# Kernel optimization log

Measured on AMD Instinct MI355X. Metric: run time of the kernel, lower is better.

## Reference

```python
import jax, jax.numpy as jnp
import numpy as np
from jax import lax

# 4D convolution via lax.conv_general_dilated (supports N spatial dims natively)
# Layout: x is (N, C, T, U, V, W); weight is (O, I, kT, kU, kV, kW)

def conv4d(x, w, b):
    dn = lax.conv_dimension_numbers(x.shape, w.shape, ('NCTUVW', 'OITUVW', 'NCTUVW'))
    y = lax.conv_general_dilated(x, w, window_strides=(1, 1, 1, 1), padding='SAME',
                                 dimension_numbers=dn)
    return y + b[None, :, None, None, None, None]


def setup_inputs() -> dict:
    key = jax.random.key(0)
    k0, k1, k2, k3, k4 = jax.random.split(key, 5)
    B, C_in, C_hid, C_out = 2, 64, 128, 64
    T, D, H, W = 4, 16, 32, 32
    K = 3  # kernel size per dim (stmode 'C' -> (3,3,3,3))
    x = jax.random.normal(k0, (B, C_in, T, D, H, W), dtype=jnp.float32)
    scale1 = 1.0 / np.sqrt(C_in * K ** 4)
    scale2 = 1.0 / np.sqrt(C_hid * K ** 4)
    w1 = jax.random.normal(k1, (C_hid, C_in, K, K, K, K), dtype=jnp.float32) * scale1
    b1 = jax.random.normal(k2, (C_hid,), dtype=jnp.float32) * scale1
    w2 = jax.random.normal(k3, (C_out, C_hid, K, K, K, K), dtype=jnp.float32) * scale2
    b2 = jax.random.normal(k4, (C_out,), dtype=jnp.float32) * scale2
    return {"x": x, "w1": w1, "b1": b1, "w2": w2, "b2": b2}


def reference(x, w1, b1, w2, b2):
    # conv1 -> ReLU -> (dropout p=0 is identity) -> conv2 -> (dropout identity)
    h = jax.nn.relu(conv4d(x, w1, b1))
    return conv4d(h, w2, b2)
```

## Files before the change

kernel.cpp:

```cpp
#include <hip/hip_runtime.h>


using bf16x8 = __attribute__((ext_vector_type(8))) __bf16;
using f32x16 = __attribute__((ext_vector_type(16))) float;
using f32x4  = __attribute__((ext_vector_type(4))) float;

typedef __attribute__((address_space(1))) const void as1_void;
typedef __attribute__((address_space(3))) void as3_void;
__device__ __forceinline__ void gload_lds16(const void* g, void* l) {
    __builtin_amdgcn_global_load_lds((as1_void*)g, (as3_void*)l, 16, 0, 0);
}

__global__ __launch_bounds__(256) void cvt_x(const float* __restrict__ x,
                                             __bf16* __restrict__ x_t,
                                             __bf16* __restrict__ zp) {
    __shared__ float lt[64][65];
    if (blockIdx.x == 0 && blockIdx.y == 0)
        *(uint4*)((char*)zp + threadIdx.x * 16) = make_uint4(0u, 0u, 0u, 0u);
    const int nb = blockIdx.y;
    const int p0 = blockIdx.x * 64;
    const int tu = p0 >> 10;
    const float* src = x + (size_t)nb * 64 * 65536;
    __bf16* dst = x_t + (size_t)nb * 65536 * 64;
    #pragma unroll
    for (int i = 0; i < 16; ++i) {
        int idx = i * 256 + threadIdx.x;
        int c = idx >> 6, p = idx & 63;
        lt[c][p] = src[(size_t)c * 65536 + p0 + p];
    }
    __syncthreads();
    #pragma unroll
    for (int it = 0; it < 2; ++it) {
        int idx = it * 256 + threadIdx.x;
        int pl = idx & 63;
        int chunk = idx >> 6;
        int p = p0 + pl;
        int v = (p >> 5) & 31, w = p & 31;
        bf16x8 pk;
        #pragma unroll
        for (int e = 0; e < 8; ++e)
            pk[e] = (__bf16)lt[chunk * 8 + e][pl];
        *(bf16x8*)(dst + (size_t)(tu * 32 + v) * 2048 + chunk * 256 + w * 8) = pk;
    }
}

template <int CIN>
__global__ __launch_bounds__(256) void cvt_w(const float* __restrict__ w,
                                             __bf16* __restrict__ wt) {
    constexpr int COUT = 8192 / CIN;
    constexpr int LOGC = (CIN == 64) ? 7 : 6;
    const int tap = blockIdx.x;
    __bf16* dst = wt + (size_t)tap * 8192;
    #pragma unroll
    for (int it = 0; it < 32; ++it) {
        const int i  = it * 256 + threadIdx.x;
        const int cl = i & 15;
        const int o  = (i >> 4) & (COUT - 1);
        const int kg = i >> (4 + LOGC);
        dst[i] = (__bf16)w[(size_t)(o * CIN + kg * 16 + cl) * 81 + tap];
    }
}

template <int CIN, int COUT, int NSPLIT, bool RELU>
__global__ __launch_bounds__(128, 2) void conv4d_mfma(
    const __bf16* __restrict__ in_t,
    const __bf16* __restrict__ wt,
    const float* __restrict__ bias,
    __bf16* __restrict__ out_bf,
    float* __restrict__ out_f,
    const __bf16* __restrict__ zpage)
{
    constexpr int KST     = CIN / 16;
    constexpr int UNITS   = CIN / 32;
    constexpr int LOGU    = (UNITS == 2) ? 1 : 2;
    constexpr int SLOTS   = 6 * 136;
    constexpr int SLOTS_P = 896;
    constexpr int RNDS    = 7;
    constexpr int BUFB_P  = SLOTS_P * 16;

    __shared__ __bf16 tile[2 * SLOTS_P * 8];

    const int tid  = threadIdx.x;
    const int lane = tid & 63;
    const int l31  = lane & 31;
    const int hl   = lane >> 5;
    const int wv   = tid >> 6;

    const int bid = blockIdx.x;
    const int xcd = bid & 7;
    const int s0  = bid >> 3;
    const int u   = xcd * 2 + (s0 & 1);
    const int vg  = (s0 >> 1) & 7;
    const int t   = (s0 >> 4) & 3;
    const int nb  = (s0 >> 6) & 1;
    const int nsp = (s0 >> 7) & (NSPLIT - 1);
    const int v0  = vg * 4;
    const int pbase = ((t * 16 + u) * 32 + v0) * 32;

    const __bf16* inb = in_t + (size_t)nb * 65536 * CIN;

    int goff[RNDS];
    #pragma unroll
    for (int r = 0; r < RNDS; ++r) {
        const int slot = r * 128 + tid;
        const int row  = slot / 136;
        const int rem  = slot - row * 136;
        const int chunk = rem / 34;
        const int wp   = rem - chunk * 34;
        const int v_in = v0 - 1 + row;
        const int w_in = wp - 1;
        const bool ok = (slot < SLOTS) && ((unsigned)v_in < 32u) &&
                        ((unsigned)w_in < 32u);
        goff[r] = ok ? (v_in * (CIN * 32) + chunk * 256 + w_in * 8) : -1;
    }

    const int lane_base = hl * 34 + l31;
    const bf16x8* tile16 = (const bf16x8*)tile;

    const int o = nsp * 64 + wv * 32 + l31;
    const __bf16* wlane = wt + (size_t)o * 16 + hl * 8;

    int sb[9], tb0[9], nst = 0;
    #pragma unroll
    for (int kt = 0; kt < 3; ++kt) {
        const int t_in = t + kt - 1;
        if ((unsigned)t_in >= 4u) continue;
        #pragma unroll
        for (int ku = 0; ku < 3; ++ku) {
            const int u_in = u + ku - 1;
            if ((unsigned)u_in >= 16u) continue;
            sb[nst]  = (t_in * 16 + u_in) * 1024 * CIN;
            tb0[nst] = (kt * 3 + ku) * 9;
            ++nst;
        }
    }
    const int U = nst * UNITS;

    f32x16 acc[4];
    #pragma unroll
    for (int mt = 0; mt < 4; ++mt)
        #pragma unroll
        for (int i = 0; i < 16; ++i)
            acc[mt][i] = 0.f;

    auto issue = [&](int buf, int j) {
        const int st = j >> LOGU, ch = j & (UNITS - 1);
        const __bf16* gb = inb + sb[st] + ch * 1024;
        char* lb = ((char*)tile) + buf * BUFB_P + wv * 1024;
        #pragma unroll
        for (int r = 0; r < RNDS; ++r) {
            const __bf16* ga = (goff[r] >= 0) ? gb + goff[r] : zpage;
            gload_lds16(ga, lb + r * 2048);
        }
    };

    auto ldA = [&](const bf16x8* tb, int g, bf16x8 (&af)[6]) {
        const int ks = g / 3, kw = g % 3;
        #pragma unroll
        for (int j = 0; j < 6; ++j)
            af[j] = tb[j * 136 + ks * 68 + kw];
    };
    auto ldB = [&](int tapb, int ch, int g, bf16x8 (&bv)[3]) {
        const int ks = g / 3, kw = g % 3;
        const int ksg = ch * 2 + ks;
        #pragma unroll
        for (int kv = 0; kv < 3; ++kv) {
            const int wo = ((tapb + kv * 3 + kw) * KST + ksg) * (COUT * 16);
            bv[kv] = *(const bf16x8*)(wlane + wo);
        }
    };
    auto mfma12 = [&](bf16x8 (&af)[6], bf16x8 (&bv)[3]) {
        #pragma unroll
        for (int kv = 0; kv < 3; ++kv)
            #pragma unroll
            for (int rr = 0; rr < 4; ++rr)
                acc[rr] = __builtin_amdgcn_mfma_f32_32x32x16_bf16(
                    af[rr + kv], bv[kv], acc[rr], 0, 0, 0);
    };

    issue(0, 0);

    #pragma unroll 1
    for (int i = 0; i < U; ++i) {
        asm volatile("s_waitcnt vmcnt(0)" ::: "memory");
        __builtin_amdgcn_s_barrier();

        const int st = i >> LOGU, ch = i & (UNITS - 1);
        const int tapb = tb0[st];
        const bf16x8* tb = tile16 + (i & 1) * SLOTS_P + lane_base;

        bf16x8 bvv[6][3];
        #pragma unroll
        for (int g = 0; g < 6; ++g)
            ldB(tapb, ch, g, bvv[g]);
        __builtin_amdgcn_sched_barrier(0);
        if (i + 1 < U) issue((i + 1) & 1, i + 1);
        __builtin_amdgcn_sched_barrier(0);

        bf16x8 afA[6], afB[6];
        ldA(tb, 0, afA);
        ldA(tb, 1, afB);
        mfma12(afA, bvv[0]);
        ldA(tb, 2, afA);
        mfma12(afB, bvv[1]);
        ldA(tb, 3, afB);
        mfma12(afA, bvv[2]);
        ldA(tb, 4, afA);
        mfma12(afB, bvv[3]);
        ldA(tb, 5, afB);
        mfma12(afA, bvv[4]);
        mfma12(afB, bvv[5]);
    }

    {
        const float bvls = bias[o];
        #pragma unroll
        for (int rr = 0; rr < 4; ++rr) {
            const int pb = pbase + rr * 32;
            if constexpr (RELU) {
                #pragma unroll
                for (int rg = 0; rg < 4; ++rg)
                    #pragma unroll
                    for (int j = 0; j < 4; ++j) {
                        float v = acc[rr][rg * 4 + j] + bvls;
                        v = v > 0.f ? v : 0.f;
                        const int p = pb + j + 8 * rg + 4 * hl;
                        const int vv = (p >> 5) & 31, ww = p & 31, tu = p >> 10;
                        out_bf[(size_t)nb * 65536 * COUT +
                               (size_t)(tu * 32 + vv) * (32 * COUT) +
                               (o >> 3) * 256 + ww * 8 + (o & 7)] = (__bf16)v;
                    }
            } else {
                #pragma unroll
                for (int rg = 0; rg < 4; ++rg) {
                    f32x4 sv;
                    #pragma unroll
                    for (int j = 0; j < 4; ++j)
                        sv[j] = acc[rr][rg * 4 + j] + bvls;
                    const int p = pb + 8 * rg + 4 * hl;
                    *(f32x4*)(out_f + ((size_t)nb * COUT + o) * 65536 + p) = sv;
                }
            }
        }
    }
}

extern "C" void kernel_launch(void* const* d_in, const int* in_sizes, int n_in,
                              void* d_out, int out_size, void* d_ws, size_t ws_size,
                              hipStream_t stream) {
    const float* x  = (const float*)d_in[0];
    const float* w1 = (const float*)d_in[1];
    const float* b1 = (const float*)d_in[2];
    const float* w2 = (const float*)d_in[3];
    const float* b2 = (const float*)d_in[4];
    float* out = (float*)d_out;

    char* ws = (char*)d_ws;
    __bf16* x_t = (__bf16*)ws;
    __bf16* h_t = (__bf16*)(ws + 16777216);
    __bf16* w1t = (__bf16*)(ws + 50331648);
    __bf16* w2t = (__bf16*)(ws + 51658752);
    __bf16* zpg = (__bf16*)(ws + 52985856);

    cvt_x<<<dim3(1024, 2), 256, 0, stream>>>(x, x_t, zpg);
    cvt_w<64><<<81, 256, 0, stream>>>(w1, w1t);
    cvt_w<128><<<81, 256, 0, stream>>>(w2, w2t);

    conv4d_mfma<64, 128, 2, true><<<2048, 128, 0, stream>>>(x_t, w1t, b1, h_t,
                                                            nullptr, zpg);
    conv4d_mfma<128, 64, 1, false><<<1024, 128, 0, stream>>>(h_t, w2t, b2,
                                                             nullptr, out, zpg);
}
```

Measured before the change: 374.1 us.

## Enlarge conv block tile to 8 v-rows, split waves over pixels not channels

Each block now covers 8 v-rows (up from 4), and the two waves split the work by pixel rows instead of by output channels. Each wave keeps 4x2 accumulator tiles, 32 rows by 64 channels, so one A fragment from LDS feeds two MFMAs and the halo overhead per block shrinks. Weight fragments are now loaded per group, interleaved with the MFMAs under explicit sched barriers. Grid sizes are halved. The cost is more accumulator registers, a larger LDS tile (occupancy risk) and fewer blocks to spread across CUs.

After: 441.2 us. 1.18x slower.

```diff
diff --git a/kernel.cpp b/kernel.cpp
--- a/kernel.cpp
+++ b/kernel.cpp
@@ -10,6 +10,7 @@
 __device__ __forceinline__ void gload_lds16(const void* g, void* l) {
     __builtin_amdgcn_global_load_lds((as1_void*)g, (as3_void*)l, 16, 0, 0);
 }
+#define SBAR() __builtin_amdgcn_sched_barrier(0)
 
 __global__ __launch_bounds__(256) void cvt_x(const float* __restrict__ x,
                                              __bf16* __restrict__ x_t,
@@ -73,9 +74,9 @@
     constexpr int KST     = CIN / 16;
     constexpr int UNITS   = CIN / 32;
     constexpr int LOGU    = (UNITS == 2) ? 1 : 2;
-    constexpr int SLOTS   = 6 * 136;
-    constexpr int SLOTS_P = 896;
-    constexpr int RNDS    = 7;
+    constexpr int SLOTS   = 10 * 136;
+    constexpr int SLOTS_P = 1408;
+    constexpr int RNDS    = 11;
     constexpr int BUFB_P  = SLOTS_P * 16;
 
     __shared__ __bf16 tile[2 * SLOTS_P * 8];
@@ -90,11 +91,11 @@
     const int xcd = bid & 7;
     const int s0  = bid >> 3;
     const int u   = xcd * 2 + (s0 & 1);
-    const int vg  = (s0 >> 1) & 7;
-    const int t   = (s0 >> 4) & 3;
-    const int nb  = (s0 >> 6) & 1;
-    const int nsp = (s0 >> 7) & (NSPLIT - 1);
-    const int v0  = vg * 4;
+    const int vg  = (s0 >> 1) & 3;
+    const int nb  = (s0 >> 3) & 1;
+    const int nsp = (NSPLIT == 2) ? ((s0 >> 4) & 1) : 0;
+    const int t   = (s0 >> ((NSPLIT == 2) ? 5 : 4)) & 3;
+    const int v0  = vg * 8;
     const int pbase = ((t * 16 + u) * 32 + v0) * 32;
 
     const __bf16* inb = in_t + (size_t)nb * 65536 * CIN;
@@ -114,11 +115,11 @@
         goff[r] = ok ? (v_in * (CIN * 32) + chunk * 256 + w_in * 8) : -1;
     }
 
-    const int lane_base = hl * 34 + l31;
+    const int lane_base = wv * 4 * 136 + hl * 34 + l31;
     const bf16x8* tile16 = (const bf16x8*)tile;
 
-    const int o = nsp * 64 + wv * 32 + l31;
-    const __bf16* wlane = wt + (size_t)o * 16 + hl * 8;
+    const int o0 = nsp * 64 + l31;
+    const __bf16* wlane = wt + (size_t)o0 * 16 + hl * 8;
 
     int sb[9], tb0[9], nst = 0;
     #pragma unroll
@@ -136,12 +137,14 @@
     }
     const int U = nst * UNITS;
 
-    f32x16 acc[4];
+    f32x16 acc[4][2];
     #pragma unroll
     for (int mt = 0; mt < 4; ++mt)
         #pragma unroll
-        for (int i = 0; i < 16; ++i)
-            acc[mt][i] = 0.f;
+        for (int nt = 0; nt < 2; ++nt)
+            #pragma unroll
+            for (int i = 0; i < 16; ++i)
+                acc[mt][nt][i] = 0.f;
 
     auto issue = [&](int buf, int j) {
         const int st = j >> LOGU, ch = j & (UNITS - 1);
@@ -160,22 +163,26 @@
         for (int j = 0; j < 6; ++j)
             af[j] = tb[j * 136 + ks * 68 + kw];
     };
-    auto ldB = [&](int tapb, int ch, int g, bf16x8 (&bv)[3]) {
+    auto ldB6 = [&](int tapb, int ch, int g, bf16x8 (&bv)[6]) {
         const int ks = g / 3, kw = g % 3;
         const int ksg = ch * 2 + ks;
         #pragma unroll
         for (int kv = 0; kv < 3; ++kv) {
             const int wo = ((tapb + kv * 3 + kw) * KST + ksg) * (COUT * 16);
-            bv[kv] = *(const bf16x8*)(wlane + wo);
-        }
-    };
-    auto mfma12 = [&](bf16x8 (&af)[6], bf16x8 (&bv)[3]) {
+            #pragma unroll
+            for (int nt = 0; nt < 2; ++nt)
+                bv[kv * 2 + nt] = *(const bf16x8*)(wlane + wo + nt * 512);
+        }
+    };
+    auto mfma24 = [&](bf16x8 (&af)[6], bf16x8 (&bv)[6]) {
         #pragma unroll
         for (int kv = 0; kv < 3; ++kv)
             #pragma unroll
-            for (int rr = 0; rr < 4; ++rr)
-                acc[rr] = __builtin_amdgcn_mfma_f32_32x32x16_bf16(
-                    af[rr + kv], bv[kv], acc[rr], 0, 0, 0);
+            for (int nt = 0; nt < 2; ++nt)
+                #pragma unroll
+                for (int rr = 0; rr < 4; ++rr)
+                    acc[rr][nt] = __builtin_amdgcn_mfma_f32_32x32x16_bf16(
+                        af[rr + kv], bv[kv * 2 + nt], acc[rr][nt], 0, 0, 0);
     };
 
     issue(0, 0);
@@ -184,45 +191,43 @@
     for (int i = 0; i < U; ++i) {
         asm volatile("s_waitcnt vmcnt(0)" ::: "memory");
         __builtin_amdgcn_s_barrier();
+        SBAR();
 
         const int st = i >> LOGU, ch = i & (UNITS - 1);
         const int tapb = tb0[st];
         const bf16x8* tb = tile16 + (i & 1) * SLOTS_P + lane_base;
 
-        bf16x8 bvv[6][3];
-        #pragma unroll
-        for (int g = 0; g < 6; ++g)
-            ldB(tapb, ch, g, bvv[g]);
-        __builtin_amdgcn_sched_barrier(0);
+        bf16x8 afA[6], afB[6], bvA[6], bvB[6];
+        ldB6(tapb, ch, 0, bvA); ldB6(tapb, ch, 1, bvB);
+        ldA(tb, 0, afA); ldA(tb, 1, afB);
+        SBAR();
+        mfma24(afA, bvA); SBAR();
+        ldA(tb, 2, afA); ldB6(tapb, ch, 2, bvA); SBAR();
+        mfma24(afB, bvB); SBAR();
+        ldA(tb, 3, afB); ldB6(tapb, ch, 3, bvB); SBAR();
+        mfma24(afA, bvA); SBAR();
+        ldA(tb, 4, afA); ldB6(tapb, ch, 4, bvA); SBAR();
+        mfma24(afB, bvB); SBAR();
+        ldA(tb, 5, afB); ldB6(tapb, ch, 5, bvB);
         if (i + 1 < U) issue((i + 1) & 1, i + 1);
-        __builtin_amdgcn_sched_barrier(0);
-
-        bf16x8 afA[6], afB[6];
-        ldA(tb, 0, afA);
-        ldA(tb, 1, afB);
-        mfma12(afA, bvv[0]);
-        ldA(tb, 2, afA);
-        mfma12(afB, bvv[1]);
-        ldA(tb, 3, afB);
-        mfma12(afA, bvv[2]);
-        ldA(tb, 4, afA);
-        mfma12(afB, bvv[3]);
-        ldA(tb, 5, afB);
-        mfma12(afA, bvv[4]);
-        mfma12(afB, bvv[5]);
-    }
-
-    {
+        SBAR();
+        mfma24(afA, bvA); SBAR();
+        mfma24(afB, bvB);
+    }
+
+    #pragma unroll
+    for (int nt = 0; nt < 2; ++nt) {
+        const int o = o0 + nt * 32;
         const float bvls = bias[o];
         #pragma unroll
         for (int rr = 0; rr < 4; ++rr) {
-            const int pb = pbase + rr * 32;
+            const int pb = pbase + (wv * 4 + rr) * 32;
             if constexpr (RELU) {
                 #pragma unroll
                 for (int rg = 0; rg < 4; ++rg)
                     #pragma unroll
                     for (int j = 0; j < 4; ++j) {
-                        float v = acc[rr][rg * 4 + j] + bvls;
+                        float v = acc[rr][nt][rg * 4 + j] + bvls;
                         v = v > 0.f ? v : 0.f;
                         const int p = pb + j + 8 * rg + 4 * hl;
                         const int vv = (p >> 5) & 31, ww = p & 31, tu = p >> 10;
@@ -236,7 +241,7 @@
                     f32x4 sv;
                     #pragma unroll
                     for (int j = 0; j < 4; ++j)
-                        sv[j] = acc[rr][rg * 4 + j] + bvls;
+                        sv[j] = acc[rr][nt][rg * 4 + j] + bvls;
                     const int p = pb + 8 * rg + 4 * hl;
                     *(f32x4*)(out_f + ((size_t)nb * COUT + o) * 65536 + p) = sv;
                 }
@@ -266,8 +271,8 @@
     cvt_w<64><<<81, 256, 0, stream>>>(w1, w1t);
     cvt_w<128><<<81, 256, 0, stream>>>(w2, w2t);
 
-    conv4d_mfma<64, 128, 2, true><<<2048, 128, 0, stream>>>(x_t, w1t, b1, h_t,
+    conv4d_mfma<64, 128, 2, true><<<1024, 128, 0, stream>>>(x_t, w1t, b1, h_t,
                                                             nullptr, zpg);
-    conv4d_mfma<128, 64, 1, false><<<1024, 128, 0, stream>>>(h_t, w2t, b2,
-                                                             nullptr, out, zpg);
-}
+    conv4d_mfma<128, 64, 1, false><<<512, 128, 0, stream>>>(h_t, w2t, b2,
+                                                            nullptr, out, zpg);
+}
```

## Halve spatial tile per block and pack stage offsets to raise occupancy

Applied to the files above, without the earlier changes.

Each conv block now covers 2 output v-rows instead of 4, so it holds two accumulator tiles instead of four and uses a smaller LDS tile. The grid doubles and launch bounds ask for 4 blocks per SM. The per-stage offset arrays are replaced by a 4-bit packed code that is decoded on the fly, which saves registers. The cost is more halo re-loading per output and the same weight-fragment loads amortised over half the MFMA work.

New measurement: 407.2 us. 1.09x slower.

```diff
diff --git a/kernel.cpp b/kernel.cpp
--- a/kernel.cpp
+++ b/kernel.cpp
@@ -10,6 +10,7 @@
 __device__ __forceinline__ void gload_lds16(const void* g, void* l) {
     __builtin_amdgcn_global_load_lds((as1_void*)g, (as3_void*)l, 16, 0, 0);
 }
+#define SBAR() __builtin_amdgcn_sched_barrier(0)
 
 __global__ __launch_bounds__(256) void cvt_x(const float* __restrict__ x,
                                              __bf16* __restrict__ x_t,
@@ -62,7 +63,7 @@
 }
 
 template <int CIN, int COUT, int NSPLIT, bool RELU>
-__global__ __launch_bounds__(128, 2) void conv4d_mfma(
+__global__ __launch_bounds__(128, 4) void conv4d_mfma(
     const __bf16* __restrict__ in_t,
     const __bf16* __restrict__ wt,
     const float* __restrict__ bias,
@@ -73,9 +74,9 @@
     constexpr int KST     = CIN / 16;
     constexpr int UNITS   = CIN / 32;
     constexpr int LOGU    = (UNITS == 2) ? 1 : 2;
-    constexpr int SLOTS   = 6 * 136;
-    constexpr int SLOTS_P = 896;
-    constexpr int RNDS    = 7;
+    constexpr int SLOTS   = 4 * 136;
+    constexpr int SLOTS_P = 640;
+    constexpr int RNDS    = 5;
     constexpr int BUFB_P  = SLOTS_P * 16;
 
     __shared__ __bf16 tile[2 * SLOTS_P * 8];
@@ -90,11 +91,11 @@
     const int xcd = bid & 7;
     const int s0  = bid >> 3;
     const int u   = xcd * 2 + (s0 & 1);
-    const int vg  = (s0 >> 1) & 7;
-    const int t   = (s0 >> 4) & 3;
-    const int nb  = (s0 >> 6) & 1;
-    const int nsp = (s0 >> 7) & (NSPLIT - 1);
-    const int v0  = vg * 4;
+    const int vg  = (s0 >> 1) & 15;
+    const int t   = (s0 >> 5) & 3;
+    const int nb  = (s0 >> 7) & 1;
+    const int nsp = (s0 >> 8) & (NSPLIT - 1);
+    const int v0  = vg * 2;
     const int pbase = ((t * 16 + u) * 32 + v0) * 32;
 
     const __bf16* inb = in_t + (size_t)nb * 65536 * CIN;
@@ -120,7 +121,8 @@
     const int o = nsp * 64 + wv * 32 + l31;
     const __bf16* wlane = wt + (size_t)o * 16 + hl * 8;
 
-    int sb[9], tb0[9], nst = 0;
+    unsigned long long pack = 0;
+    int nst = 0;
     #pragma unroll
     for (int kt = 0; kt < 3; ++kt) {
         const int t_in = t + kt - 1;
@@ -129,23 +131,26 @@
         for (int ku = 0; ku < 3; ++ku) {
             const int u_in = u + ku - 1;
             if ((unsigned)u_in >= 16u) continue;
-            sb[nst]  = (t_in * 16 + u_in) * 1024 * CIN;
-            tb0[nst] = (kt * 3 + ku) * 9;
+            pack |= (unsigned long long)(kt * 3 + ku) << (4 * nst);
             ++nst;
         }
     }
     const int U = nst * UNITS;
-
-    f32x16 acc[4];
-    #pragma unroll
-    for (int mt = 0; mt < 4; ++mt)
+    auto stage_sb = [&](int code) {
+        const int kt = (code * 11) >> 5;
+        const int ku = code - kt * 3;
+        return ((t + kt - 1) * 16 + (u + ku - 1)) * 1024 * CIN;
+    };
+
+    f32x16 acc[2];
+    #pragma unroll
+    for (int mt = 0; mt < 2; ++mt)
         #pragma unroll
         for (int i = 0; i < 16; ++i)
             acc[mt][i] = 0.f;
 
-    auto issue = [&](int buf, int j) {
-        const int st = j >> LOGU, ch = j & (UNITS - 1);
-        const __bf16* gb = inb + sb[st] + ch * 1024;
+    auto issue = [&](int buf, int sbv, int ch) {
+        const __bf16* gb = inb + sbv + ch * 1024;
         char* lb = ((char*)tile) + buf * BUFB_P + wv * 1024;
         #pragma unroll
         for (int r = 0; r < RNDS; ++r) {
@@ -154,10 +159,10 @@
         }
     };
 
-    auto ldA = [&](const bf16x8* tb, int g, bf16x8 (&af)[6]) {
+    auto ldA = [&](const bf16x8* tb, int g, bf16x8 (&af)[4]) {
         const int ks = g / 3, kw = g % 3;
         #pragma unroll
-        for (int j = 0; j < 6; ++j)
+        for (int j = 0; j < 4; ++j)
             af[j] = tb[j * 136 + ks * 68 + kw];
     };
     auto ldB = [&](int tapb, int ch, int g, bf16x8 (&bv)[3]) {
@@ -169,53 +174,57 @@
             bv[kv] = *(const bf16x8*)(wlane + wo);
         }
     };
-    auto mfma12 = [&](bf16x8 (&af)[6], bf16x8 (&bv)[3]) {
+    auto mfma6 = [&](bf16x8 (&af)[4], bf16x8 (&bv)[3]) {
         #pragma unroll
         for (int kv = 0; kv < 3; ++kv)
             #pragma unroll
-            for (int rr = 0; rr < 4; ++rr)
+            for (int rr = 0; rr < 2; ++rr)
                 acc[rr] = __builtin_amdgcn_mfma_f32_32x32x16_bf16(
                     af[rr + kv], bv[kv], acc[rr], 0, 0, 0);
     };
 
-    issue(0, 0);
+    issue(0, stage_sb((int)(pack & 15)), 0);
 
     #pragma unroll 1
     for (int i = 0; i < U; ++i) {
         asm volatile("s_waitcnt vmcnt(0)" ::: "memory");
         __builtin_amdgcn_s_barrier();
 
-        const int st = i >> LOGU, ch = i & (UNITS - 1);
-        const int tapb = tb0[st];
+        const int st   = i >> LOGU, ch = i & (UNITS - 1);
+        const int code = (int)((pack >> (st * 4)) & 15);
+        const int tapb = code * 9;
         const bf16x8* tb = tile16 + (i & 1) * SLOTS_P + lane_base;
 
         bf16x8 bvv[6][3];
         #pragma unroll
         for (int g = 0; g < 6; ++g)
             ldB(tapb, ch, g, bvv[g]);
-        __builtin_amdgcn_sched_barrier(0);
-        if (i + 1 < U) issue((i + 1) & 1, i + 1);
-        __builtin_amdgcn_sched_barrier(0);
-
-        bf16x8 afA[6], afB[6];
+        SBAR();
+        if (i + 1 < U) {
+            const int ncode = (int)((pack >> (((i + 1) >> LOGU) * 4)) & 15);
+            issue((i + 1) & 1, stage_sb(ncode), (i + 1) & (UNITS - 1));
+        }
+        SBAR();
+
+        bf16x8 afA[4], afB[4];
         ldA(tb, 0, afA);
         ldA(tb, 1, afB);
-        mfma12(afA, bvv[0]);
+        mfma6(afA, bvv[0]);
         ldA(tb, 2, afA);
-        mfma12(afB, bvv[1]);
+        mfma6(afB, bvv[1]);
         ldA(tb, 3, afB);
-        mfma12(afA, bvv[2]);
+        mfma6(afA, bvv[2]);
         ldA(tb, 4, afA);
-        mfma12(afB, bvv[3]);
+        mfma6(afB, bvv[3]);
         ldA(tb, 5, afB);
-        mfma12(afA, bvv[4]);
-        mfma12(afB, bvv[5]);
+        mfma6(afA, bvv[4]);
+        mfma6(afB, bvv[5]);
     }
 
     {
         const float bvls = bias[o];
         #pragma unroll
-        for (int rr = 0; rr < 4; ++rr) {
+        for (int rr = 0; rr < 2; ++rr) {
             const int pb = pbase + rr * 32;
             if constexpr (RELU) {
                 #pragma unroll
@@ -266,8 +275,8 @@
     cvt_w<64><<<81, 256, 0, stream>>>(w1, w1t);
     cvt_w<128><<<81, 256, 0, stream>>>(w2, w2t);
 
-    conv4d_mfma<64, 128, 2, true><<<2048, 128, 0, stream>>>(x_t, w1t, b1, h_t,
+    conv4d_mfma<64, 128, 2, true><<<4096, 128, 0, stream>>>(x_t, w1t, b1, h_t,
                                                             nullptr, zpg);
-    conv4d_mfma<128, 64, 1, false><<<1024, 128, 0, stream>>>(h_t, w2t, b2,
+    conv4d_mfma<128, 64, 1, false><<<2048, 128, 0, stream>>>(h_t, w2t, b2,
                                                              nullptr, out, zpg);
 }
```
